# Optimization experiments

Hardware: AMD Instinct MI355X
Metric: run time of the kernel (lower is better)

Reference implementation:

```python
import jax, jax.numpy as jnp
import numpy as np

B, S, D, H = 1, 2048, 1024, 16
DH = D // H  # 64
HID = 4 * D
EPS = 1e-5
NEG = -1.0e9


def setup_inputs() -> dict:
    key = jax.random.key(0)
    ks = jax.random.split(key, 12)
    s = 0.02
    return {
        "y": jax.random.normal(ks[0], (B, S, D), jnp.float32),
        "encoder_output": jax.random.normal(ks[1], (B, S, D), jnp.float32),
        # per-head shared projection (query_fc used for q,k,v — faithful to source bug)
        "Wq_self": jax.random.normal(ks[2], (H, D, DH), jnp.float32) * s,
        "bq_self": jax.random.normal(ks[3], (H, DH), jnp.float32) * s,
        "Wq_cross": jax.random.normal(ks[4], (H, D, DH), jnp.float32) * s,
        "bq_cross": jax.random.normal(ks[5], (H, DH), jnp.float32) * s,
        "g1": jnp.ones((D,), jnp.float32), "beta1": jnp.zeros((D,), jnp.float32),
        "g2": jnp.ones((D,), jnp.float32), "beta2": jnp.zeros((D,), jnp.float32),
        "g3": jnp.ones((D,), jnp.float32), "beta3": jnp.zeros((D,), jnp.float32),
        "w1": jax.random.normal(ks[6], (D, HID), jnp.float32) * s,
        "b1": jax.random.normal(ks[7], (HID,), jnp.float32) * s,
        "w2": jax.random.normal(ks[8], (HID, D), jnp.float32) * s,
        "b2": jax.random.normal(ks[9], (D,), jnp.float32) * s,
    }


def _layernorm(x, g, b):
    mu = jnp.mean(x, axis=-1, keepdims=True)
    var = jnp.mean((x - mu) ** 2, axis=-1, keepdims=True)
    return (x - mu) * jax.lax.rsqrt(var + EPS) * g + b


def _mha(x_q, x_kv, W, bias, causal):
    # source bug: q, k, v all use query_fc projection
    q = jnp.einsum('bsd,hde->bhse', x_q, W) + bias[None, :, None, :]
    k = jnp.einsum('bsd,hde->bhse', x_kv, W) + bias[None, :, None, :]
    v = jnp.einsum('bsd,hde->bhse', x_kv, W) + bias[None, :, None, :]
    scores = jnp.einsum('bhse,bhte->bhst', q, k) / jnp.sqrt(jnp.float32(DH))
    if causal:
        sq, sk = scores.shape[-2], scores.shape[-1]
        mask = jnp.triu(jnp.ones((sq, sk), bool), k=1)
        scores = jnp.where(mask, NEG, scores)
    p = jax.nn.softmax(scores, axis=-1)
    out = jnp.einsum('bhst,bhte->bhse', p, v)  # [B,H,S,DH]
    b, h, s, e = out.shape
    return out.transpose(0, 2, 1, 3).reshape(b, s, h * e)


def reference(y, encoder_output, Wq_self, bq_self, Wq_cross, bq_cross,
              g1, beta1, g2, beta2, g3, beta3, w1, b1, w2, b2):
    sa = _mha(y, y, Wq_self, bq_self, causal=True)
    y1 = _layernorm(y + sa, g1, beta1)
    ca = _mha(y1, encoder_output, Wq_cross, bq_cross, causal=False)
    y2 = _layernorm(y1 + ca, g2, beta2)
    ff = jnp.maximum(y2 @ w1 + b1, 0.0) @ w2 + b2
    return _layernorm(y2 + ff, g3, beta3)
```

## Files before the change

### kernel.cpp

```cpp
#include <hip/hip_runtime.h>
#include <hip/hip_bf16.h>


#define S_LEN 2048
#define DMODEL 1024
#define NHEAD 16
#define DHEAD 64
#define HIDDEN 4096

using bf16 = __hip_bfloat16;
typedef __attribute__((ext_vector_type(8))) short bf16x8;
typedef __attribute__((ext_vector_type(4))) float floatx4;

__device__ __forceinline__ void async_ld16(const void* g, void* l) {
  __builtin_amdgcn_global_load_lds(
      (const __attribute__((address_space(1))) unsigned int*)g,
      (__attribute__((address_space(3))) unsigned int*)l, 16, 0, 0);
}

__device__ __forceinline__ unsigned short f2bf_bits(float f) {
  __hip_bfloat16 b = __float2bfloat16(f);
  return *(unsigned short*)&b;
}

template <bool HEADB>
__global__ __launch_bounds__(256) void transp_bf16_kernel(
    const float* __restrict__ src0, bf16* __restrict__ dst0,
    const float* __restrict__ src1, bf16* __restrict__ dst1, int K, int N) {
  const float* src = blockIdx.z ? src1 : src0;
  bf16* dst = blockIdx.z ? dst1 : dst0;
  __shared__ float tile[32][33];
  const int tx = threadIdx.x & 31, ty = threadIdx.x >> 5;
  const int k0 = blockIdx.y * 32, n0 = blockIdx.x * 32;
#pragma unroll
  for (int i = 0; i < 4; ++i) {
    const int k = k0 + ty + i * 8;
    const int n = n0 + tx;
    size_t idx;
    if (HEADB)
      idx = (size_t)(n >> 6) * ((size_t)K * 64) + (size_t)k * 64 + (n & 63);
    else
      idx = (size_t)k * N + n;
    tile[ty + i * 8][tx] = src[idx];
  }
  __syncthreads();
#pragma unroll
  for (int i = 0; i < 4; ++i) {
    const int n = n0 + ty + i * 8;
    const int k = k0 + tx;
    dst[(size_t)n * K + k] = __float2bfloat16(tile[tx][ty + i * 8]);
  }
}

__global__ __launch_bounds__(256) void conv_bf16_kernel(
    const float* __restrict__ src0, bf16* __restrict__ dst0,
    const float* __restrict__ src1, bf16* __restrict__ dst1, int n4) {
  const float* src = blockIdx.z ? src1 : src0;
  bf16* dst = blockIdx.z ? dst1 : dst0;
  const int i = blockIdx.x * 256 + threadIdx.x;
  if (i >= n4) return;
  float4 v = ((const float4*)src)[i];
  unsigned short r[4] = {f2bf_bits(v.x), f2bf_bits(v.y), f2bf_bits(v.z), f2bf_bits(v.w)};
  ((ushort2*)dst)[i * 2] = make_ushort2(r[0], r[1]);
  ((ushort2*)dst)[i * 2 + 1] = make_ushort2(r[2], r[3]);
}

template <int BM, int BN, bool RELU, bool DUALT, typename CT>
__global__ __launch_bounds__(256) void mfma_gemm_kernel(
    const bf16* __restrict__ A0, const bf16* __restrict__ Bt0,
    const float* __restrict__ bias0, CT* __restrict__ C0,
    bf16* __restrict__ Ct0,
    const bf16* __restrict__ A1, const bf16* __restrict__ Bt1,
    const float* __restrict__ bias1, CT* __restrict__ C1,
    bf16* __restrict__ Ct1,
    int M, int N, int Kstride, int Klen) {
  const bf16* A = blockIdx.z ? A1 : A0;
  const bf16* Bt = blockIdx.z ? Bt1 : Bt0;
  const float* bias = blockIdx.z ? bias1 : bias0;
  CT* C = blockIdx.z ? C1 : C0;
  bf16* Ct = blockIdx.z ? Ct1 : Ct0;

  constexpr int MF = BM / 32;
  constexpr int NF = BN / 32;
  __shared__ __align__(16) bf16 As[BM * 32];
  __shared__ __align__(16) bf16 Bs[BN * 32];

  const int tid = threadIdx.x;
  const int wave = tid >> 6;
  const int lane = tid & 63;
  const int m0 = blockIdx.y * BM;
  const int n0 = blockIdx.x * BN;
  const int wr = wave >> 1, wc = wave & 1;

  const int srow = wave * 16 + (lane >> 2);
  const int skcol = (lane & 3) * 8;
  const bf16* agp = A + (size_t)(m0 + srow) * Kstride + skcol;
  const bf16* bgp = Bt + (size_t)(n0 + srow) * Kstride + skcol;
  char* alds = (char*)As + wave * 1024;
  char* blds = (char*)Bs + wave * 1024;

  floatx4 acc[MF][NF];
#pragma unroll
  for (int i = 0; i < MF; ++i)
#pragma unroll
    for (int j = 0; j < NF; ++j) acc[i][j] = floatx4{0.f, 0.f, 0.f, 0.f};

  const int mrow = lane & 15;
  const int kqb = (lane >> 4) * 16;

  for (int kt = 0; kt < Klen; kt += 32) {
    __syncthreads();
#pragma unroll
    for (int i = 0; i < BM / 64; ++i)
      async_ld16(agp + (size_t)(i * 64) * Kstride + kt, alds + i * 4096);
#pragma unroll
    for (int i = 0; i < BN / 64; ++i)
      async_ld16(bgp + (size_t)(i * 64) * Kstride + kt, blds + i * 4096);
    __syncthreads();

    bf16x8 af[MF], bfr[NF];
#pragma unroll
    for (int fi = 0; fi < MF; ++fi)
      af[fi] = *(const bf16x8*)((char*)As + (wr * (BM / 2) + fi * 16 + mrow) * 64 + kqb);
#pragma unroll
    for (int fj = 0; fj < NF; ++fj)
      bfr[fj] = *(const bf16x8*)((char*)Bs + (wc * (BN / 2) + fj * 16 + mrow) * 64 + kqb);
#pragma unroll
    for (int fi = 0; fi < MF; ++fi)
#pragma unroll
      for (int fj = 0; fj < NF; ++fj)
        acc[fi][fj] = __builtin_amdgcn_mfma_f32_16x16x32_bf16(
            af[fi], bfr[fj], acc[fi][fj], 0, 0, 0);
  }

  const int erow = (lane >> 4) * 4;
  const int ecol = lane & 15;
#pragma unroll
  for (int fi = 0; fi < MF; ++fi) {
#pragma unroll
    for (int fj = 0; fj < NF; ++fj) {
      const int nn = n0 + wc * (BN / 2) + fj * 16 + ecol;
      const float bv = bias ? bias[nn] : 0.0f;
      const int mmb = m0 + wr * (BM / 2) + fi * 16 + erow;
      float v[4];
#pragma unroll
      for (int r = 0; r < 4; ++r) {
        v[r] = acc[fi][fj][r] + bv;
        if (RELU) v[r] = fmaxf(v[r], 0.0f);
        if constexpr (sizeof(CT) == 2)
          C[(size_t)(mmb + r) * N + nn] = (CT)__float2bfloat16(v[r]);
        else
          C[(size_t)(mmb + r) * N + nn] = (CT)v[r];
      }
      if (DUALT) {
        ushort4 pk;
        pk.x = f2bf_bits(v[0]);
        pk.y = f2bf_bits(v[1]);
        pk.z = f2bf_bits(v[2]);
        pk.w = f2bf_bits(v[3]);
        *(ushort4*)&Ct[(size_t)nn * M + mmb] = pk;
      }
    }
  }
}

__global__ __launch_bounds__(256) void mfma_attn_kernel(
    const bf16* __restrict__ Q, const bf16* __restrict__ K,
    const bf16* __restrict__ Vt,
    float* __restrict__ OA, float* __restrict__ OB,
    float* __restrict__ LA, float* __restrict__ LB, int causal) {
  __shared__ __align__(16) unsigned short Kt[64 * 64];
  __shared__ __align__(16) unsigned short Vs[64 * 64];
  __shared__ unsigned short Ps[4][16][72];

  const int tid = threadIdx.x;
  const int w = tid >> 6, lane = tid & 63;
  const int g = lane >> 4, c = lane & 15;
  const int h = blockIdx.y;
  const int q0 = blockIdx.x * 64;
  const int z = blockIdx.z;
  const int qw = q0 + w * 16;
  float* Oz = z ? OB : OA;
  float* Lz = z ? LB : LA;

  const bf16* qrow = Q + (size_t)(qw + c) * DMODEL + h * DHEAD + g * 8;
  const bf16x8 qf0 = *(const bf16x8*)qrow;
  const bf16x8 qf1 = *(const bf16x8*)(qrow + 32);

  const int srow = tid >> 3;
  const int schunk = (tid & 7) ^ (srow & 7);
  const bf16* kgp = K + (size_t)srow * DMODEL + h * DHEAD + schunk * 8;
  const bf16* vgp = Vt + (size_t)(h * DHEAD + srow) * S_LEN + schunk * 8;
  char* klds = (char*)Kt + w * 1024;
  char* vlds = (char*)Vs + w * 1024;

  const int kpos0 = ((g ^ (c & 7)) << 4);
  const int kpos1 = kpos0 ^ 64;

  floatx4 of[4];
#pragma unroll
  for (int md = 0; md < 4; ++md) of[md] = floatx4{0.f, 0.f, 0.f, 0.f};
  float lpart = 0.0f;

  const int nkt = causal ? (q0 / 64 + 1) : (S_LEN / 64);
  for (int kt = z; kt < nkt; kt += 2) {
    const int t0 = kt * 64;

    __syncthreads();
    async_ld16(kgp + (size_t)t0 * DMODEL, klds);
    async_ld16(kgp + (size_t)(t0 + 32) * DMODEL, klds + 4096);
    async_ld16(vgp + t0, vlds);
    async_ld16(vgp + (size_t)32 * S_LEN + t0, vlds + 4096);
    __syncthreads();

    const bool diag = causal && (t0 == q0);
#pragma unroll
    for (int jt = 0; jt < 4; ++jt) {
      const char* kr = (const char*)Kt + (16 * jt + c) * 128;
      const bf16x8 kf0 = *(const bf16x8*)(kr + kpos0);
      const bf16x8 kf1 = *(const bf16x8*)(kr + kpos1);
      floatx4 s = floatx4{0.f, 0.f, 0.f, 0.f};
      s = __builtin_amdgcn_mfma_f32_16x16x32_bf16(kf0, qf0, s, 0, 0, 0);
      s = __builtin_amdgcn_mfma_f32_16x16x32_bf16(kf1, qf1, s, 0, 0, 0);

      ushort4 pk;
      unsigned short* pp = (unsigned short*)&pk;
#pragma unroll
      for (int r = 0; r < 4; ++r) {
        float p = __expf(0.125f * s[r]);
        if (diag && (t0 + 16 * jt + 4 * g + r > qw + c)) p = 0.0f;
        lpart += p;
        pp[r] = f2bf_bits(p);
      }
      *(ushort4*)&Ps[w][c][16 * jt + 4 * g] = pk;
    }

#pragma unroll
    for (int ks = 0; ks < 2; ++ks) {
      const bf16x8 pf = *(const bf16x8*)&Ps[w][c][32 * ks + 8 * g];
      const int vpos = ks ? kpos1 : kpos0;
#pragma unroll
      for (int md = 0; md < 4; ++md) {
        const bf16x8 vf =
            *(const bf16x8*)((const char*)Vs + (md * 16 + c) * 128 + vpos);
        of[md] = __builtin_amdgcn_mfma_f32_16x16x32_bf16(vf, pf, of[md], 0, 0, 0);
      }
    }
  }

  lpart += __shfl_xor(lpart, 16, 64);
  lpart += __shfl_xor(lpart, 32, 64);
  if (g == 0) Lz[(size_t)h * S_LEN + qw + c] = lpart;

  float* orow = Oz + (size_t)(qw + c) * DMODEL + h * DHEAD;
#pragma unroll
  for (int md = 0; md < 4; ++md) {
    float4 v;
    v.x = of[md][0];
    v.y = of[md][1];
    v.z = of[md][2];
    v.w = of[md][3];
    *(float4*)(orow + md * 16 + 4 * g) = v;
  }
}

template <bool DUAL, bool MERGE, bool SUM2>
__global__ __launch_bounds__(256) void add_ln_kernel(
    const float* __restrict__ X, const float* __restrict__ R,
    const float* __restrict__ R2, const float* __restrict__ bvec,
    const float* __restrict__ La, const float* __restrict__ Lb,
    const float* __restrict__ g, const float* __restrict__ beta,
    float* __restrict__ out, bf16* __restrict__ out2) {
  const int row = blockIdx.x;
  const int tid = threadIdx.x;

  float v[4];
  float s1 = 0.0f, s2 = 0.0f;
#pragma unroll
  for (int i = 0; i < 4; ++i) {
    const int c = tid + i * 256;
    float x = X[(size_t)row * DMODEL + c];
    if (MERGE) {
      const int h = c >> 6;
      const float rl =
          1.0f / (La[(size_t)h * S_LEN + row] + Lb[(size_t)h * S_LEN + row]);
      x += (R[(size_t)row * DMODEL + c] + R2[(size_t)row * DMODEL + c]) * rl;
    } else if (SUM2) {
      x += R[(size_t)row * DMODEL + c] + R2[(size_t)row * DMODEL + c] + bvec[c];
    } else {
      x += R[(size_t)row * DMODEL + c];
    }
    v[i] = x;
    s1 += x;
    s2 += x * x;
  }
#pragma unroll
  for (int off = 32; off; off >>= 1) {
    s1 += __shfl_xor(s1, off, 64);
    s2 += __shfl_xor(s2, off, 64);
  }
  __shared__ float w1s[4], w2s[4];
  const int wid = tid >> 6, lane = tid & 63;
  if (lane == 0) { w1s[wid] = s1; w2s[wid] = s2; }
  __syncthreads();
  s1 = w1s[0] + w1s[1] + w1s[2] + w1s[3];
  s2 = w2s[0] + w2s[1] + w2s[2] + w2s[3];

  const float mu = s1 * (1.0f / DMODEL);
  const float var = s2 * (1.0f / DMODEL) - mu * mu;
  const float rstd = rsqrtf(var + 1e-5f);

#pragma unroll
  for (int i = 0; i < 4; ++i) {
    const int c = tid + i * 256;
    const float r = (v[i] - mu) * rstd * g[c] + beta[c];
    out[(size_t)row * DMODEL + c] = r;
    if (DUAL) out2[(size_t)row * DMODEL + c] = __float2bfloat16(r);
  }
}

extern "C" void kernel_launch(void* const* d_in, const int* in_sizes, int n_in,
                              void* d_out, int out_size, void* d_ws, size_t ws_size,
                              hipStream_t stream) {
  const float* y      = (const float*)d_in[0];
  const float* enc    = (const float*)d_in[1];
  const float* Wself  = (const float*)d_in[2];
  const float* bself  = (const float*)d_in[3];
  const float* Wcross = (const float*)d_in[4];
  const float* bcross = (const float*)d_in[5];
  const float* g1     = (const float*)d_in[6];
  const float* be1    = (const float*)d_in[7];
  const float* g2     = (const float*)d_in[8];
  const float* be2    = (const float*)d_in[9];
  const float* g3     = (const float*)d_in[10];
  const float* be3    = (const float*)d_in[11];
  const float* w1     = (const float*)d_in[12];
  const float* b1     = (const float*)d_in[13];
  const float* w2     = (const float*)d_in[14];
  const float* b2     = (const float*)d_in[15];
  float* out = (float*)d_out;

  char* ws = (char*)d_ws;
  const size_t MB = 1024 * 1024;
  bf16*  ybf   = (bf16*)(ws + 0 * MB);
  bf16*  encbf = (bf16*)(ws + 4 * MB);
  float* PA    = (float*)(ws + 0 * MB);
  float* PB    = (float*)(ws + 8 * MB);
  float* Y1    = (float*)(ws + 16 * MB);
  float* Y2    = (float*)(ws + 24 * MB);
  bf16*  Q12b  = (bf16*)(ws + 32 * MB);
  bf16*  Q1t   = (bf16*)(ws + 36 * MB);
  bf16*  K2b   = (bf16*)(ws + 40 * MB);
  bf16*  K2t   = (bf16*)(ws + 44 * MB);
  bf16*  w1t   = (bf16*)(ws + 48 * MB);
  bf16*  w2t   = (bf16*)(ws + 56 * MB);
  bf16*  Wst   = (bf16*)(ws + 64 * MB);
  bf16*  Wct   = (bf16*)(ws + 66 * MB);
  bf16*  Y1bf  = (bf16*)(ws + 68 * MB);
  bf16*  Y2bf  = (bf16*)(ws + 72 * MB);
  float* La    = (float*)(ws + 76 * MB);
  float* Lb    = (float*)(ws + 76 * MB + 512 * 1024);
  bf16*  FFH   = (bf16*)(ws + 0 * MB);
  float* FFa   = (float*)(ws + 32 * MB);
  float* FFb   = (float*)(ws + 40 * MB);

  const dim3 blk(256);
  const dim3 gT_w(DMODEL / 32, DMODEL / 32, 2);
  const dim3 gT_w1(HIDDEN / 32, DMODEL / 32);
  const dim3 gT_w2(DMODEL / 32, HIDDEN / 32);
  const dim3 gConv(S_LEN * DMODEL / 4 / 256, 1, 2);
  const dim3 gProj2(DMODEL / 64, S_LEN / 64, 2);
  const dim3 gProj(DMODEL / 64, S_LEN / 64);
  const dim3 gFf1(HIDDEN / 128, S_LEN / 64);
  const dim3 gFf2(DMODEL / 64, S_LEN / 64, 2);
  const dim3 gAttn(S_LEN / 64, NHEAD, 2);
  const dim3 gLn(S_LEN);

  transp_bf16_kernel<true><<<gT_w, blk, 0, stream>>>(
      Wself, Wst, Wcross, Wct, DMODEL, DMODEL);
  transp_bf16_kernel<false><<<gT_w1, blk, 0, stream>>>(
      w1, w1t, nullptr, nullptr, DMODEL, HIDDEN);
  transp_bf16_kernel<false><<<gT_w2, blk, 0, stream>>>(
      w2, w2t, nullptr, nullptr, HIDDEN, DMODEL);
  conv_bf16_kernel<<<gConv, blk, 0, stream>>>(
      y, ybf, enc, encbf, S_LEN * DMODEL / 4);

  mfma_gemm_kernel<64, 64, false, true, bf16><<<gProj2, blk, 0, stream>>>(
      ybf, Wst, bself, Q12b, Q1t,
      encbf, Wct, bcross, K2b, K2t, S_LEN, DMODEL, DMODEL, DMODEL);
  mfma_attn_kernel<<<gAttn, blk, 0, stream>>>(
      Q12b, Q12b, Q1t, PA, PB, La, Lb, 1);
  add_ln_kernel<true, true, false><<<gLn, blk, 0, stream>>>(
      y, PA, PB, nullptr, La, Lb, g1, be1, Y1, Y1bf);
  mfma_gemm_kernel<64, 64, false, false, bf16><<<gProj, blk, 0, stream>>>(
      Y1bf, Wct, bcross, Q12b, nullptr,
      nullptr, nullptr, nullptr, nullptr, nullptr, S_LEN, DMODEL, DMODEL, DMODEL);
  mfma_attn_kernel<<<gAttn, blk, 0, stream>>>(
      Q12b, K2b, K2t, PA, PB, La, Lb, 0);
  add_ln_kernel<true, true, false><<<gLn, blk, 0, stream>>>(
      Y1, PA, PB, nullptr, La, Lb, g2, be2, Y2, Y2bf);
  mfma_gemm_kernel<64, 128, true, false, bf16><<<gFf1, blk, 0, stream>>>(
      Y2bf, w1t, b1, FFH, nullptr,
      nullptr, nullptr, nullptr, nullptr, nullptr, S_LEN, HIDDEN, DMODEL, DMODEL);
  mfma_gemm_kernel<64, 64, false, false, float><<<gFf2, blk, 0, stream>>>(
      FFH, w2t, nullptr, FFa, nullptr,
      FFH + HIDDEN / 2, w2t + HIDDEN / 2, nullptr, FFb, nullptr,
      S_LEN, DMODEL, HIDDEN, HIDDEN / 2);
  add_ln_kernel<false, false, true><<<gLn, blk, 0, stream>>>(
      Y2, FFa, FFb, b2, nullptr, nullptr, g3, be3, out, nullptr);
}
```

Baseline: 325.7 us.

## Deepen GEMM K-tile to 64 with swizzled LDS; widen attention waves to 32 queries

The GEMM kernel now stages 64-wide K slices per iteration using an XOR-swizzled LDS layout and issues two MFMAs per fragment pair, halving the barrier count and avoiding bank conflicts. The attention kernel switches to 128-thread blocks where each wave handles 32 query rows, so every K/V fragment read from LDS is reused across two MFMA streams. This raises register use and LDS footprint per block and halves the waves per attention block, which may reduce latency hiding.

```diff
diff --git a/kernel.cpp b/kernel.cpp
--- a/kernel.cpp
+++ b/kernel.cpp
@@ -82,8 +82,8 @@
 
   constexpr int MF = BM / 32;
   constexpr int NF = BN / 32;
-  __shared__ __align__(16) bf16 As[BM * 32];
-  __shared__ __align__(16) bf16 Bs[BN * 32];
+  __shared__ __align__(16) bf16 As[BM * 64];
+  __shared__ __align__(16) bf16 Bs[BN * 64];
 
   const int tid = threadIdx.x;
   const int wave = tid >> 6;
@@ -92,10 +92,10 @@
   const int n0 = blockIdx.x * BN;
   const int wr = wave >> 1, wc = wave & 1;
 
-  const int srow = wave * 16 + (lane >> 2);
-  const int skcol = (lane & 3) * 8;
-  const bf16* agp = A + (size_t)(m0 + srow) * Kstride + skcol;
-  const bf16* bgp = Bt + (size_t)(n0 + srow) * Kstride + skcol;
+  const int srow = tid >> 3;
+  const int schunk = (tid & 7) ^ (srow & 7);
+  const bf16* agp = A + (size_t)(m0 + srow) * Kstride + schunk * 8;
+  const bf16* bgp = Bt + (size_t)(n0 + srow) * Kstride + schunk * 8;
   char* alds = (char*)As + wave * 1024;
   char* blds = (char*)Bs + wave * 1024;
 
@@ -106,31 +106,41 @@
     for (int j = 0; j < NF; ++j) acc[i][j] = floatx4{0.f, 0.f, 0.f, 0.f};
 
   const int mrow = lane & 15;
-  const int kqb = (lane >> 4) * 16;
-
-  for (int kt = 0; kt < Klen; kt += 32) {
+  const int p0 = (((lane >> 4) ^ (mrow & 7)) << 4);
+  const int p1 = p0 ^ 64;
+
+  for (int kt = 0; kt < Klen; kt += 64) {
     __syncthreads();
 #pragma unroll
-    for (int i = 0; i < BM / 64; ++i)
-      async_ld16(agp + (size_t)(i * 64) * Kstride + kt, alds + i * 4096);
-#pragma unroll
-    for (int i = 0; i < BN / 64; ++i)
-      async_ld16(bgp + (size_t)(i * 64) * Kstride + kt, blds + i * 4096);
+    for (int i = 0; i < BM / 32; ++i)
+      async_ld16(agp + (size_t)(32 * i) * Kstride + kt, alds + i * 4096);
+#pragma unroll
+    for (int i = 0; i < BN / 32; ++i)
+      async_ld16(bgp + (size_t)(32 * i) * Kstride + kt, blds + i * 4096);
     __syncthreads();
 
-    bf16x8 af[MF], bfr[NF];
+    bf16x8 af0[MF], af1[MF], bf0[NF], bf1[NF];
+#pragma unroll
+    for (int fi = 0; fi < MF; ++fi) {
+      const char* ar = (char*)As + (wr * (BM / 2) + fi * 16 + mrow) * 128;
+      af0[fi] = *(const bf16x8*)(ar + p0);
+      af1[fi] = *(const bf16x8*)(ar + p1);
+    }
+#pragma unroll
+    for (int fj = 0; fj < NF; ++fj) {
+      const char* br = (char*)Bs + (wc * (BN / 2) + fj * 16 + mrow) * 128;
+      bf0[fj] = *(const bf16x8*)(br + p0);
+      bf1[fj] = *(const bf16x8*)(br + p1);
+    }
 #pragma unroll
     for (int fi = 0; fi < MF; ++fi)
-      af[fi] = *(const bf16x8*)((char*)As + (wr * (BM / 2) + fi * 16 + mrow) * 64 + kqb);
-#pragma unroll
-    for (int fj = 0; fj < NF; ++fj)
-      bfr[fj] = *(const bf16x8*)((char*)Bs + (wc * (BN / 2) + fj * 16 + mrow) * 64 + kqb);
-#pragma unroll
-    for (int fi = 0; fi < MF; ++fi)
-#pragma unroll
-      for (int fj = 0; fj < NF; ++fj)
+#pragma unroll
+      for (int fj = 0; fj < NF; ++fj) {
         acc[fi][fj] = __builtin_amdgcn_mfma_f32_16x16x32_bf16(
-            af[fi], bfr[fj], acc[fi][fj], 0, 0, 0);
+            af0[fi], bf0[fj], acc[fi][fj], 0, 0, 0);
+        acc[fi][fj] = __builtin_amdgcn_mfma_f32_16x16x32_bf16(
+            af1[fi], bf1[fj], acc[fi][fj], 0, 0, 0);
+      }
   }
 
   const int erow = (lane >> 4) * 4;
@@ -164,14 +174,14 @@
   }
 }
 
-__global__ __launch_bounds__(256) void mfma_attn_kernel(
+__global__ __launch_bounds__(128) void mfma_attn_kernel(
     const bf16* __restrict__ Q, const bf16* __restrict__ K,
     const bf16* __restrict__ Vt,
     float* __restrict__ OA, float* __restrict__ OB,
     float* __restrict__ LA, float* __restrict__ LB, int causal) {
   __shared__ __align__(16) unsigned short Kt[64 * 64];
   __shared__ __align__(16) unsigned short Vs[64 * 64];
-  __shared__ unsigned short Ps[4][16][72];
+  __shared__ unsigned short Ps[2][32][72];
 
   const int tid = threadIdx.x;
   const int w = tid >> 6, lane = tid & 63;
@@ -179,13 +189,18 @@
   const int h = blockIdx.y;
   const int q0 = blockIdx.x * 64;
   const int z = blockIdx.z;
-  const int qw = q0 + w * 16;
+  const int qw = q0 + w * 32;
   float* Oz = z ? OB : OA;
   float* Lz = z ? LB : LA;
 
-  const bf16* qrow = Q + (size_t)(qw + c) * DMODEL + h * DHEAD + g * 8;
-  const bf16x8 qf0 = *(const bf16x8*)qrow;
-  const bf16x8 qf1 = *(const bf16x8*)(qrow + 32);
+  bf16x8 qf0[2], qf1[2];
+#pragma unroll
+  for (int qs = 0; qs < 2; ++qs) {
+    const bf16* qrow =
+        Q + (size_t)(qw + qs * 16 + c) * DMODEL + h * DHEAD + g * 8;
+    qf0[qs] = *(const bf16x8*)qrow;
+    qf1[qs] = *(const bf16x8*)(qrow + 32);
+  }
 
   const int srow = tid >> 3;
   const int schunk = (tid & 7) ^ (srow & 7);
@@ -197,20 +212,23 @@
   const int kpos0 = ((g ^ (c & 7)) << 4);
   const int kpos1 = kpos0 ^ 64;
 
-  floatx4 of[4];
-#pragma unroll
-  for (int md = 0; md < 4; ++md) of[md] = floatx4{0.f, 0.f, 0.f, 0.f};
-  float lpart = 0.0f;
+  floatx4 of[4][2];
+#pragma unroll
+  for (int md = 0; md < 4; ++md)
+#pragma unroll
+    for (int qs = 0; qs < 2; ++qs) of[md][qs] = floatx4{0.f, 0.f, 0.f, 0.f};
+  float lpart[2] = {0.f, 0.f};
 
   const int nkt = causal ? (q0 / 64 + 1) : (S_LEN / 64);
   for (int kt = z; kt < nkt; kt += 2) {
     const int t0 = kt * 64;
 
     __syncthreads();
-    async_ld16(kgp + (size_t)t0 * DMODEL, klds);
-    async_ld16(kgp + (size_t)(t0 + 32) * DMODEL, klds + 4096);
-    async_ld16(vgp + t0, vlds);
-    async_ld16(vgp + (size_t)32 * S_LEN + t0, vlds + 4096);
+#pragma unroll
+    for (int i = 0; i < 4; ++i) {
+      async_ld16(kgp + (size_t)(t0 + 16 * i) * DMODEL, klds + i * 2048);
+      async_ld16(vgp + (size_t)(16 * i) * S_LEN + t0, vlds + i * 2048);
+    }
     __syncthreads();
 
     const bool diag = causal && (t0 == q0);
@@ -219,48 +237,55 @@
       const char* kr = (const char*)Kt + (16 * jt + c) * 128;
       const bf16x8 kf0 = *(const bf16x8*)(kr + kpos0);
       const bf16x8 kf1 = *(const bf16x8*)(kr + kpos1);
-      floatx4 s = floatx4{0.f, 0.f, 0.f, 0.f};
-      s = __builtin_amdgcn_mfma_f32_16x16x32_bf16(kf0, qf0, s, 0, 0, 0);
-      s = __builtin_amdgcn_mfma_f32_16x16x32_bf16(kf1, qf1, s, 0, 0, 0);
-
-      ushort4 pk;
-      unsigned short* pp = (unsigned short*)&pk;
-#pragma unroll
-      for (int r = 0; r < 4; ++r) {
-        float p = __expf(0.125f * s[r]);
-        if (diag && (t0 + 16 * jt + 4 * g + r > qw + c)) p = 0.0f;
-        lpart += p;
-        pp[r] = f2bf_bits(p);
+#pragma unroll
+      for (int qs = 0; qs < 2; ++qs) {
+        floatx4 s = floatx4{0.f, 0.f, 0.f, 0.f};
+        s = __builtin_amdgcn_mfma_f32_16x16x32_bf16(kf0, qf0[qs], s, 0, 0, 0);
+        s = __builtin_amdgcn_mfma_f32_16x16x32_bf16(kf1, qf1[qs], s, 0, 0, 0);
+
+        ushort4 pk;
+        unsigned short* pp = (unsigned short*)&pk;
+#pragma unroll
+        for (int r = 0; r < 4; ++r) {
+          float p = __expf(0.125f * s[r]);
+          if (diag && (t0 + 16 * jt + 4 * g + r > qw + qs * 16 + c)) p = 0.0f;
+          lpart[qs] += p;
+          pp[r] = f2bf_bits(p);
+        }
+        *(ushort4*)&Ps[w][qs * 16 + c][16 * jt + 4 * g] = pk;
       }
-      *(ushort4*)&Ps[w][c][16 * jt + 4 * g] = pk;
     }
 
 #pragma unroll
     for (int ks = 0; ks < 2; ++ks) {
-      const bf16x8 pf = *(const bf16x8*)&Ps[w][c][32 * ks + 8 * g];
+      const bf16x8 pf0 = *(const bf16x8*)&Ps[w][c][32 * ks + 8 * g];
+      const bf16x8 pf1 = *(const bf16x8*)&Ps[w][16 + c][32 * ks + 8 * g];
       const int vpos = ks ? kpos1 : kpos0;
 #pragma unroll
       for (int md = 0; md < 4; ++md) {
         const bf16x8 vf =
             *(const bf16x8*)((const char*)Vs + (md * 16 + c) * 128 + vpos);
-        of[md] = __builtin_amdgcn_mfma_f32_16x16x32_bf16(vf, pf, of[md], 0, 0, 0);
+        of[md][0] = __builtin_amdgcn_mfma_f32_16x16x32_bf16(vf, pf0, of[md][0], 0, 0, 0);
+        of[md][1] = __builtin_amdgcn_mfma_f32_16x16x32_bf16(vf, pf1, of[md][1], 0, 0, 0);
       }
     }
   }
 
-  lpart += __shfl_xor(lpart, 16, 64);
-  lpart += __shfl_xor(lpart, 32, 64);
-  if (g == 0) Lz[(size_t)h * S_LEN + qw + c] = lpart;
-
-  float* orow = Oz + (size_t)(qw + c) * DMODEL + h * DHEAD;
-#pragma unroll
-  for (int md = 0; md < 4; ++md) {
-    float4 v;
-    v.x = of[md][0];
-    v.y = of[md][1];
-    v.z = of[md][2];
-    v.w = of[md][3];
-    *(float4*)(orow + md * 16 + 4 * g) = v;
+#pragma unroll
+  for (int qs = 0; qs < 2; ++qs) {
+    lpart[qs] += __shfl_xor(lpart[qs], 16, 64);
+    lpart[qs] += __shfl_xor(lpart[qs], 32, 64);
+    if (g == 0) Lz[(size_t)h * S_LEN + qw + qs * 16 + c] = lpart[qs];
+    float* orow = Oz + (size_t)(qw + qs * 16 + c) * DMODEL + h * DHEAD;
+#pragma unroll
+    for (int md = 0; md < 4; ++md) {
+      float4 v;
+      v.x = of[md][qs][0];
+      v.y = of[md][qs][1];
+      v.z = of[md][qs][2];
+      v.w = of[md][qs][3];
+      *(float4*)(orow + md * 16 + 4 * g) = v;
+    }
   }
 }
 
@@ -365,6 +390,7 @@
   float* FFb   = (float*)(ws + 40 * MB);
 
   const dim3 blk(256);
+  const dim3 blkA(128);
   const dim3 gT_w(DMODEL / 32, DMODEL / 32, 2);
   const dim3 gT_w1(HIDDEN / 32, DMODEL / 32);
   const dim3 gT_w2(DMODEL / 32, HIDDEN / 32);
@@ -388,14 +414,14 @@
   mfma_gemm_kernel<64, 64, false, true, bf16><<<gProj2, blk, 0, stream>>>(
       ybf, Wst, bself, Q12b, Q1t,
       encbf, Wct, bcross, K2b, K2t, S_LEN, DMODEL, DMODEL, DMODEL);
-  mfma_attn_kernel<<<gAttn, blk, 0, stream>>>(
+  mfma_attn_kernel<<<gAttn, blkA, 0, stream>>>(
       Q12b, Q12b, Q1t, PA, PB, La, Lb, 1);
   add_ln_kernel<true, true, false><<<gLn, blk, 0, stream>>>(
       y, PA, PB, nullptr, La, Lb, g1, be1, Y1, Y1bf);
   mfma_gemm_kernel<64, 64, false, false, bf16><<<gProj, blk, 0, stream>>>(
       Y1bf, Wct, bcross, Q12b, nullptr,
       nullptr, nullptr, nullptr, nullptr, nullptr, S_LEN, DMODEL, DMODEL, DMODEL);
-  mfma_attn_kernel<<<gAttn, blk, 0, stream>>>(
+  mfma_attn_kernel<<<gAttn, blkA, 0, stream>>>(
       Q12b, K2b, K2t, PA, PB, La, Lb, 0);
   add_ln_kernel<true, true, false><<<gLn, blk, 0, stream>>>(
       Y1, PA, PB, nullptr, La, Lb, g2, be2, Y2, Y2bf);
```

Measured after the change: 317.1 us. 1.03x faster.
